# Kernel optimization log

Measured on AMD Instinct MI355X. Metric: run time of the kernel, lower is better.

Reference implementation:

```python
import math
import jax, jax.numpy as jnp
import numpy as np

B, N, DIN, DOUT = 64, 512, 256, 256
EPS = 1e-5  # torch BatchNorm1d default


def setup_inputs() -> dict:
    key = jax.random.key(0)
    k0, k1, k2, k3 = jax.random.split(key, 4)
    x = jax.random.normal(k0, (B, N, DIN), dtype=jnp.float32)
    # row-scaled dense adjacency (keeps activation magnitudes sane)
    adj = jax.random.uniform(k1, (B, N, N), dtype=jnp.float32) / N
    # prefix-style masks: first L_i nodes of each graph are valid
    lengths = jax.random.randint(k2, (B,), N // 4, N + 1)
    mask = (jnp.arange(N)[None, :] < lengths[:, None]).astype(jnp.float32)
    # xavier_normal_ init for weight
    std = math.sqrt(2.0 / (DIN + DOUT))
    weight = jax.random.normal(k3, (DIN, DOUT), dtype=jnp.float32) * std
    bias = jnp.zeros((DOUT,), dtype=jnp.float32)
    gamma = jnp.ones((DOUT,), dtype=jnp.float32)   # BN affine scale
    beta = jnp.zeros((DOUT,), dtype=jnp.float32)   # BN affine shift
    return {"x": x, "adj": adj, "mask": mask, "weight": weight,
            "bias": bias, "gamma": gamma, "beta": beta}


def reference(x, adj, mask, weight, bias, gamma, beta):
    # y = adj @ x @ W + b
    y = jnp.einsum('bnm,bmd->bnd', adj, x)
    y = jnp.einsum('bnd,de->bne', y, weight) + bias
    # masked BatchNorm1d (training mode): batch stats over all valid nodes,
    # equivalent to the torch code's pack -> BN -> unpack on prefix masks.
    m = mask[:, :, None]                       # [B, N, 1]
    n = jnp.sum(mask)                          # total valid nodes
    mean = jnp.sum(y * m, axis=(0, 1)) / n     # [DOUT]
    var = jnp.sum(((y - mean) ** 2) * m, axis=(0, 1)) / n  # biased var
    y = ((y - mean) * jax.lax.rsqrt(var + EPS) * gamma + beta) * m
    return jax.nn.relu(y)
```

## Files before the change

### kernel.cpp

```cpp
#include <hip/hip_runtime.h>

#define B_    64
#define N_    512
#define DIN_  256
#define DOUT_ 256
#define EPS_  1e-5f
#define ROWS_ (B_ * N_)
#define NBLK_Y2 512

typedef __attribute__((ext_vector_type(8))) short bf16x8;
typedef __attribute__((ext_vector_type(8))) unsigned short u16x8;
typedef __attribute__((ext_vector_type(4))) float f32x4;
typedef __attribute__((ext_vector_type(4))) short short4v;

__device__ __forceinline__ short f2bf(float f) {
    unsigned u = __builtin_bit_cast(unsigned, f);
    u += 0x7fff + ((u >> 16) & 1);
    return (short)(u >> 16);
}

__device__ __forceinline__ void gload_lds16(const void* g, void* l) {
    __builtin_amdgcn_global_load_lds(
        (const __attribute__((address_space(1))) void*)g,
        (__attribute__((address_space(3))) void*)l, 16, 0, 0);
}


__global__ __launch_bounds__(256) void wt_cvt(const float* __restrict__ W,
                                              short* __restrict__ WTf) {
    const int c = blockIdx.x * 256 + threadIdx.x;
    const int kf = c >> 10, ef = (c >> 6) & 15, lp = c & 63;
    const int e = ef * 16 + (lp & 15);
    const int k0 = kf * 32 + (lp >> 4) * 8;
    bf16x8 h;
    #pragma unroll
    for (int j = 0; j < 8; ++j)
        h[j] = f2bf(W[(size_t)(k0 + j) * DOUT_ + e]);
    *(bf16x8*)&WTf[(size_t)c * 8] = h;
}

__global__ __launch_bounds__(512, 4) void gemm_xw(const float* __restrict__ X,
                                                  const short* __restrict__ WTf,
                                                  short* __restrict__ xwT) {
    __shared__ __align__(16) short Bs[2][16384];
    __shared__ __align__(16) short As[2][4096];
    const int tid = threadIdx.x, wv = tid >> 6, lane = tid & 63;
    const int lrow = lane & 15, lg = lane >> 4;
    const int bid = blockIdx.x;
    const int rowBase = bid * 64;

    const int s_row = ((tid >> 6) & 3) * 16 + (tid & 15);
    const int s_kloc = (tid >> 8) * 32 + ((tid >> 4) & 3) * 8;
    const float* Xr = &X[(size_t)(rowBase + s_row) * DIN_ + s_kloc];

    f32x4 acc[4][2] = {};
    float4 av0, av1;

    av0 = *(const float4*)(Xr);
    av1 = *(const float4*)(Xr + 4);
    #pragma unroll
    for (int j = 0; j < 4; ++j) {
        int o = tid * 16 + j * 8192;
        gload_lds16((const char*)WTf + o, (char*)&Bs[0][0] + o);
    }
    {
        bf16x8 h = { f2bf(av0.x), f2bf(av0.y), f2bf(av0.z), f2bf(av0.w),
                     f2bf(av1.x), f2bf(av1.y), f2bf(av1.z), f2bf(av1.w) };
        *(bf16x8*)((char*)&As[0][0] + tid * 16) = h;
    }
    __syncthreads();

    int cur = 0;
    for (int c = 0; c < 4; ++c) {
        if (c < 3) {
            av0 = *(const float4*)(Xr + (c + 1) * 64);
            av1 = *(const float4*)(Xr + (c + 1) * 64 + 4);
            #pragma unroll
            for (int j = 0; j < 4; ++j) {
                int o = tid * 16 + j * 8192;
                gload_lds16((const char*)WTf + (c + 1) * 32768 + o,
                            (char*)&Bs[cur ^ 1][0] + o);
            }
        }
        #pragma unroll
        for (int kf2 = 0; kf2 < 2; ++kf2) {
            bf16x8 a[4], b[2];
            #pragma unroll
            for (int m = 0; m < 4; ++m)
                a[m] = *(const bf16x8*)((char*)&As[cur][0] +
                                        ((kf2 * 4 + m) * 64 + lane) * 16);
            #pragma unroll
            for (int nf = 0; nf < 2; ++nf)
                b[nf] = *(const bf16x8*)((char*)&Bs[cur][0] +
                                         ((kf2 * 16 + wv * 2 + nf) * 64 + lane) * 16);
            #pragma unroll
            for (int m = 0; m < 4; ++m)
                #pragma unroll
                for (int nf = 0; nf < 2; ++nf)
                    acc[m][nf] = __builtin_amdgcn_mfma_f32_16x16x32_bf16(
                        a[m], b[nf], acc[m][nf], 0, 0, 0);
        }
        if (c < 3) {
            bf16x8 h = { f2bf(av0.x), f2bf(av0.y), f2bf(av0.z), f2bf(av0.w),
                         f2bf(av1.x), f2bf(av1.y), f2bf(av1.z), f2bf(av1.w) };
            *(bf16x8*)((char*)&As[cur ^ 1][0] + tid * 16) = h;
        }
        __syncthreads();
        cur ^= 1;
    }

    const int bz = bid >> 3, kfbase = (bid & 7) * 2;
    short* xwb = xwT + (size_t)bz * 131072;
    #pragma unroll
    for (int m = 0; m < 4; ++m)
        #pragma unroll
        for (int nf = 0; nf < 2; ++nf) {
            int kf = kfbase + (m >> 1);
            int ef = wv * 2 + nf;
            int lanep = lrow + 16 * ((m & 1) * 2 + (lg >> 1));
            size_t off = ((size_t)(kf * 16 + ef) * 64 + lanep) * 8 + (lg & 1) * 4;
            short4v o = { f2bf(acc[m][nf][0]), f2bf(acc[m][nf][1]),
                          f2bf(acc[m][nf][2]), f2bf(acc[m][nf][3]) };
            *(short4v*)&xwb[off] = o;
        }
}

template <bool BF16Y2>
__global__ __launch_bounds__(512, 4) void gemm_y2(const float* __restrict__ adj,
                                                  const short* __restrict__ xwT,
                                                  const float* __restrict__ bias,
                                                  const float* __restrict__ mask,
                                                  float* __restrict__ outf,
                                                  unsigned short* __restrict__ y2b,
                                                  float* __restrict__ psum,
                                                  float* __restrict__ psumsq,
                                                  float* __restrict__ pcnt) {
    __shared__ __align__(16) short Bs[4][8192];
    __shared__ __align__(16) short As[2][2048];
    const int tid = threadIdx.x, wv = tid >> 6, lane = tid & 63;
    const int lrow = lane & 15, lg = lane >> 4;
    const int bid = blockIdx.x;
    const int swz = ((bid & 7) << 6) | (bid >> 3);
    const int bz = swz >> 3, mt = swz & 7;
    const int rowBase = mt * 64;
    const float* A = adj + (size_t)bz * N_ * N_;
    const short* xwb = xwT + (size_t)bz * 131072;

    const int arow = ((tid >> 7) << 4) | ((tid >> 1) & 15);
    const int akl  = (((tid >> 5) & 3) << 3) | ((tid & 1) << 2);
    const float* Ar = &A[(size_t)(rowBase + arow) * N_ + akl];

    float4 av[2];
    f32x4 acc[4][2] = {};

    float4 av0t = *(const float4*)(Ar);
    av[1] = *(const float4*)(Ar + 32);
    __builtin_amdgcn_sched_barrier(0);
    #pragma unroll
    for (int p = 0; p < 3; ++p) {
        const char* src = (const char*)xwb + p * 16384;
        char* dst = (char*)&Bs[p][0];
        gload_lds16(src + tid * 16, dst + tid * 16);
        gload_lds16(src + tid * 16 + 8192, dst + tid * 16 + 8192);
    }
    __builtin_amdgcn_sched_barrier(0);
    {
        short4v h = { f2bf(av0t.x), f2bf(av0t.y), f2bf(av0t.z), f2bf(av0t.w) };
        *(short4v*)((char*)&As[0][0] + tid * 8) = h;
    }
    asm volatile("s_waitcnt lgkmcnt(0)" ::: "memory");
    asm volatile("s_waitcnt vmcnt(4)" ::: "memory");
    __builtin_amdgcn_s_barrier();
    asm volatile("" ::: "memory");

    #pragma unroll 1
    for (int cc = 0; cc < 16; cc += 4) {
        #pragma unroll
        for (int u = 0; u < 4; ++u) {
            const int c = cc + u;
            {
                const int cn = (c + 2 < 16) ? c + 2 : 15;
                av[c & 1] = *(const float4*)(Ar + cn * 32);
            }
            __builtin_amdgcn_sched_barrier(0);
            {
                const int cn = (c + 3 < 16) ? c + 3 : 15;
                const char* src = (const char*)xwb + cn * 16384;
                char* dst = (char*)&Bs[(c + 3) & 3][0];
                gload_lds16(src + tid * 16, dst + tid * 16);
                gload_lds16(src + tid * 16 + 8192, dst + tid * 16 + 8192);
            }
            __builtin_amdgcn_sched_barrier(0);
            {
                const char* ab = (const char*)&As[c & 1][0];
                const char* bb = (const char*)&Bs[c & 3][0];
                bf16x8 a0 = *(const bf16x8*)(ab + (0 * 64 + lane) * 16);
                bf16x8 a1 = *(const bf16x8*)(ab + (1 * 64 + lane) * 16);
                bf16x8 a2 = *(const bf16x8*)(ab + (2 * 64 + lane) * 16);
                bf16x8 a3 = *(const bf16x8*)(ab + (3 * 64 + lane) * 16);
                bf16x8 b0 = *(const bf16x8*)(bb + ((wv * 2 + 0) * 64 + lane) * 16);
                bf16x8 b1 = *(const bf16x8*)(bb + ((wv * 2 + 1) * 64 + lane) * 16);
                acc[0][0] = __builtin_amdgcn_mfma_f32_16x16x32_bf16(a0, b0, acc[0][0], 0, 0, 0);
                acc[0][1] = __builtin_amdgcn_mfma_f32_16x16x32_bf16(a0, b1, acc[0][1], 0, 0, 0);
                acc[1][0] = __builtin_amdgcn_mfma_f32_16x16x32_bf16(a1, b0, acc[1][0], 0, 0, 0);
                acc[1][1] = __builtin_amdgcn_mfma_f32_16x16x32_bf16(a1, b1, acc[1][1], 0, 0, 0);
                acc[2][0] = __builtin_amdgcn_mfma_f32_16x16x32_bf16(a2, b0, acc[2][0], 0, 0, 0);
                acc[2][1] = __builtin_amdgcn_mfma_f32_16x16x32_bf16(a2, b1, acc[2][1], 0, 0, 0);
                acc[3][0] = __builtin_amdgcn_mfma_f32_16x16x32_bf16(a3, b0, acc[3][0], 0, 0, 0);
                acc[3][1] = __builtin_amdgcn_mfma_f32_16x16x32_bf16(a3, b1, acc[3][1], 0, 0, 0);
            }
            __builtin_amdgcn_sched_barrier(0);
            {
                float4 v = av[(c + 1) & 1];
                short4v h = { f2bf(v.x), f2bf(v.y), f2bf(v.z), f2bf(v.w) };
                *(short4v*)((char*)&As[(c + 1) & 1][0] + tid * 8) = h;
            }
            asm volatile("s_waitcnt lgkmcnt(0)" ::: "memory");
            asm volatile("s_waitcnt vmcnt(5)" ::: "memory");
            __builtin_amdgcn_s_barrier();
            asm volatile("" ::: "memory");
        }
    }

    float* C = outf + (size_t)bz * N_ * DOUT_;
    unsigned short* Cb = y2b + (size_t)bz * N_ * DOUT_;
    float mv[4][4];
    #pragma unroll
    for (int m = 0; m < 4; ++m)
        #pragma unroll
        for (int r = 0; r < 4; ++r)
            mv[m][r] = mask[bz * N_ + rowBase + m * 16 + lg * 4 + r];
    float sv[2] = {0.f, 0.f}, sq[2] = {0.f, 0.f};
    #pragma unroll
    for (int nf = 0; nf < 2; ++nf) {
        const int col = wv * 32 + nf * 16 + lrow;
        const float bv = bias[col];
        #pragma unroll
        for (int m = 0; m < 4; ++m) {
            const int r0 = rowBase + m * 16 + lg * 4;
            #pragma unroll
            for (int r = 0; r < 4; ++r) {
                float v = acc[m][nf][r] + bv;
                if (BF16Y2)
                    Cb[(size_t)(r0 + r) * DOUT_ + col] = (unsigned short)f2bf(v);
                else
                    C[(size_t)(r0 + r) * DOUT_ + col] = v;
                float vm = v * mv[m][r];
                sv[nf] += vm;
                sq[nf] = fmaf(v, vm, sq[nf]);
            }
        }
    }
    #pragma unroll
    for (int nf = 0; nf < 2; ++nf) {
        sv[nf] += __shfl_xor(sv[nf], 16); sv[nf] += __shfl_xor(sv[nf], 32);
        sq[nf] += __shfl_xor(sq[nf], 16); sq[nf] += __shfl_xor(sq[nf], 32);
    }
    const int pidx = bz * 8 + mt;
    if (lg == 0) {
        #pragma unroll
        for (int nf = 0; nf < 2; ++nf) {
            psum[(size_t)pidx * DOUT_ + wv * 32 + nf * 16 + lrow]   = sv[nf];
            psumsq[(size_t)pidx * DOUT_ + wv * 32 + nf * 16 + lrow] = sq[nf];
        }
    }
    if (wv == 0) {
        float cnt = mask[bz * N_ + rowBase + lane];
        #pragma unroll
        for (int i = 1; i < 64; i <<= 1) cnt += __shfl_xor(cnt, i);
        if (lane == 0) pcnt[pidx] = cnt;
    }
}

__global__ __launch_bounds__(256) void finalize2(const float* __restrict__ psum,
                                                 const float* __restrict__ psumsq,
                                                 const float* __restrict__ pcnt,
                                                 const float* __restrict__ gamma,
                                                 const float* __restrict__ beta,
                                                 float* __restrict__ scsh) {
    const int e = blockIdx.x, t = threadIdx.x;
    float s  = psum[(size_t)t * DOUT_ + e]   + psum[(size_t)(t + 256) * DOUT_ + e];
    float ss = psumsq[(size_t)t * DOUT_ + e] + psumsq[(size_t)(t + 256) * DOUT_ + e];
    float n  = pcnt[t] + pcnt[t + 256];
    #pragma unroll
    for (int i = 1; i < 64; i <<= 1) {
        s += __shfl_xor(s, i); ss += __shfl_xor(ss, i); n += __shfl_xor(n, i);
    }
    __shared__ float red[3][4];
    const int wv = t >> 6;
    if ((t & 63) == 0) { red[0][wv] = s; red[1][wv] = ss; red[2][wv] = n; }
    __syncthreads();
    if (t == 0) {
        s  = red[0][0] + red[0][1] + red[0][2] + red[0][3];
        ss = red[1][0] + red[1][1] + red[1][2] + red[1][3];
        n  = red[2][0] + red[2][1] + red[2][2] + red[2][3];
        float mean = s / n;
        float var = ss / n - mean * mean;
        float sc = rsqrtf(var + EPS_) * gamma[e];
        scsh[e] = sc;
        scsh[DOUT_ + e] = beta[e] - mean * sc;
    }
}

__global__ __launch_bounds__(256) void norm_relu_bf(const unsigned short* __restrict__ y2b,
                                                    const float* __restrict__ mask,
                                                    const float* __restrict__ scsh,
                                                    float* __restrict__ out) {
    const int nq = ROWS_ * (DOUT_ / 8);
    for (int q = blockIdx.x * blockDim.x + threadIdx.x; q < nq;
         q += gridDim.x * blockDim.x) {
        int e8 = (q & 31) * 8;
        int r = q >> 5;
        float m = mask[r];
        u16x8 uv = *(const u16x8*)&y2b[(size_t)q * 8];
        float4 sc0 = *(const float4*)&scsh[e8];
        float4 sc1 = *(const float4*)&scsh[e8 + 4];
        float4 sh0 = *(const float4*)&scsh[DOUT_ + e8];
        float4 sh1 = *(const float4*)&scsh[DOUT_ + e8 + 4];
        float4 o0, o1;
        #pragma unroll
        for (int j = 0; j < 4; ++j) {
            float f = __builtin_bit_cast(float, (unsigned)uv[j] << 16);
            (&o0.x)[j] = fmaxf(fmaf(f, (&sc0.x)[j], (&sh0.x)[j]) * m, 0.f);
        }
        #pragma unroll
        for (int j = 0; j < 4; ++j) {
            float f = __builtin_bit_cast(float, (unsigned)uv[j + 4] << 16);
            (&o1.x)[j] = fmaxf(fmaf(f, (&sc1.x)[j], (&sh1.x)[j]) * m, 0.f);
        }
        *(float4*)&out[(size_t)q * 8] = o0;
        *(float4*)&out[(size_t)q * 8 + 4] = o1;
    }
}

__global__ __launch_bounds__(256) void norm_relu_f32(float* __restrict__ y2,
                                                     const float* __restrict__ mask,
                                                     const float* __restrict__ scsh) {
    const int nq = ROWS_ * (DOUT_ / 4);
    for (int q = blockIdx.x * blockDim.x + threadIdx.x; q < nq;
         q += gridDim.x * blockDim.x) {
        int e4 = (q & 63) * 4;
        int r = q >> 6;
        float m = mask[r];
        float4 v  = *(float4*)&y2[(size_t)q * 4];
        float4 sc = *(const float4*)&scsh[e4];
        float4 sh = *(const float4*)&scsh[DOUT_ + e4];
        v.x = fmaxf(fmaf(v.x, sc.x, sh.x) * m, 0.f);
        v.y = fmaxf(fmaf(v.y, sc.y, sh.y) * m, 0.f);
        v.z = fmaxf(fmaf(v.z, sc.z, sh.z) * m, 0.f);
        v.w = fmaxf(fmaf(v.w, sc.w, sh.w) * m, 0.f);
        *(float4*)&y2[(size_t)q * 4] = v;
    }
}

extern "C" void kernel_launch(void* const* d_in, const int* in_sizes, int n_in,
                              void* d_out, int out_size, void* d_ws, size_t ws_size,
                              hipStream_t stream) {
    const float* x      = (const float*)d_in[0];
    const float* adj    = (const float*)d_in[1];
    const float* mask   = (const float*)d_in[2];
    const float* weight = (const float*)d_in[3];
    const float* bias   = (const float*)d_in[4];
    const float* gamma  = (const float*)d_in[5];
    const float* beta   = (const float*)d_in[6];
    float* out = (float*)d_out;

    const size_t xw_elems = (size_t)DOUT_ * ROWS_;
    const size_t need_bf = 131072 + xw_elems * 2 * 2 +
                           (size_t)NBLK_Y2 * DOUT_ * 4 * 2 + NBLK_Y2 * 4 + 2048 + 64;
    const bool use_bf = ws_size >= need_bf;

    short* WTf    = (short*)d_ws;
    short* xwT    = WTf + 256 * 256;
    unsigned short* y2b = (unsigned short*)(xwT + xw_elems);
    float* psum   = use_bf ? (float*)(y2b + xw_elems) : (float*)(y2b);
    float* psumsq = psum + NBLK_Y2 * DOUT_;
    float* pcnt   = psumsq + NBLK_Y2 * DOUT_;
    float* scsh   = pcnt + NBLK_Y2;

    wt_cvt<<<32, 256, 0, stream>>>(weight, WTf);
    gemm_xw<<<512, 512, 0, stream>>>(x, WTf, xwT);
    if (use_bf) {
        gemm_y2<true><<<NBLK_Y2, 512, 0, stream>>>(adj, xwT, bias, mask, out, y2b,
                                                   psum, psumsq, pcnt);
        finalize2<<<256, 256, 0, stream>>>(psum, psumsq, pcnt, gamma, beta, scsh);
        norm_relu_bf<<<2048, 256, 0, stream>>>(y2b, mask, scsh, out);
    } else {
        gemm_y2<false><<<NBLK_Y2, 512, 0, stream>>>(adj, xwT, bias, mask, out, y2b,
                                                    psum, psumsq, pcnt);
        finalize2<<<256, 256, 0, stream>>>(psum, psumsq, pcnt, gamma, beta, scsh);
        norm_relu_f32<<<2048, 256, 0, stream>>>(out, mask, scsh);
    }
}
```

Before: 55.20 us.

## Stage full A tile in LDS upfront and stream B fragments directly from global

Both GEMM kernels now convert and load the entire A row-block (X or adj) into LDS once, with one barrier. B fragments (weights / xw) are then read straight from global memory into registers, one step ahead, instead of going through async LDS staging. This removes the per-step barriers and LDS traffic for B. In exchange it loses the overlap of A loads with compute, and the larger LDS footprint (64KB in gemm_y2) may limit occupancy.

```diff
diff --git a/kernel.cpp b/kernel.cpp
--- a/kernel.cpp
+++ b/kernel.cpp
@@ -19,12 +19,6 @@
     return (short)(u >> 16);
 }
 
-__device__ __forceinline__ void gload_lds16(const void* g, void* l) {
-    __builtin_amdgcn_global_load_lds(
-        (const __attribute__((address_space(1))) void*)g,
-        (__attribute__((address_space(3))) void*)l, 16, 0, 0);
-}
-
 
 __global__ __launch_bounds__(256) void wt_cvt(const float* __restrict__ W,
                                               short* __restrict__ WTf) {
@@ -42,71 +36,51 @@
 __global__ __launch_bounds__(512, 4) void gemm_xw(const float* __restrict__ X,
                                                   const short* __restrict__ WTf,
                                                   short* __restrict__ xwT) {
-    __shared__ __align__(16) short Bs[2][16384];
-    __shared__ __align__(16) short As[2][4096];
+    __shared__ __align__(16) short As[8 * 4 * 64 * 8];
     const int tid = threadIdx.x, wv = tid >> 6, lane = tid & 63;
     const int lrow = lane & 15, lg = lane >> 4;
     const int bid = blockIdx.x;
     const int rowBase = bid * 64;
 
-    const int s_row = ((tid >> 6) & 3) * 16 + (tid & 15);
-    const int s_kloc = (tid >> 8) * 32 + ((tid >> 4) & 3) * 8;
-    const float* Xr = &X[(size_t)(rowBase + s_row) * DIN_ + s_kloc];
-
+    #pragma unroll
+    for (int j = 0; j < 4; ++j) {
+        int s = tid + j * 512;
+        int kf = s >> 8, mf = (s >> 6) & 3, lp = s & 63;
+        int row = mf * 16 + (lp & 15);
+        int k = kf * 32 + (lp >> 4) * 8;
+        const float* src = &X[(size_t)(rowBase + row) * DIN_ + k];
+        float4 v0 = *(const float4*)src;
+        float4 v1 = *(const float4*)(src + 4);
+        bf16x8 h = { f2bf(v0.x), f2bf(v0.y), f2bf(v0.z), f2bf(v0.w),
+                     f2bf(v1.x), f2bf(v1.y), f2bf(v1.z), f2bf(v1.w) };
+        *(bf16x8*)&As[s * 8] = h;
+    }
+    __syncthreads();
+
+    const short* b0p = WTf + ((size_t)(wv * 2 + 0) * 64 + lane) * 8;
+    const short* b1p = WTf + ((size_t)(wv * 2 + 1) * 64 + lane) * 8;
+    bf16x8 bc0 = *(const bf16x8*)(b0p);
+    bf16x8 bc1 = *(const bf16x8*)(b1p);
     f32x4 acc[4][2] = {};
-    float4 av0, av1;
-
-    av0 = *(const float4*)(Xr);
-    av1 = *(const float4*)(Xr + 4);
-    #pragma unroll
-    for (int j = 0; j < 4; ++j) {
-        int o = tid * 16 + j * 8192;
-        gload_lds16((const char*)WTf + o, (char*)&Bs[0][0] + o);
-    }
-    {
-        bf16x8 h = { f2bf(av0.x), f2bf(av0.y), f2bf(av0.z), f2bf(av0.w),
-                     f2bf(av1.x), f2bf(av1.y), f2bf(av1.z), f2bf(av1.w) };
-        *(bf16x8*)((char*)&As[0][0] + tid * 16) = h;
-    }
-    __syncthreads();
-
-    int cur = 0;
-    for (int c = 0; c < 4; ++c) {
-        if (c < 3) {
-            av0 = *(const float4*)(Xr + (c + 1) * 64);
-            av1 = *(const float4*)(Xr + (c + 1) * 64 + 4);
-            #pragma unroll
-            for (int j = 0; j < 4; ++j) {
-                int o = tid * 16 + j * 8192;
-                gload_lds16((const char*)WTf + (c + 1) * 32768 + o,
-                            (char*)&Bs[cur ^ 1][0] + o);
-            }
-        }
-        #pragma unroll
-        for (int kf2 = 0; kf2 < 2; ++kf2) {
-            bf16x8 a[4], b[2];
-            #pragma unroll
-            for (int m = 0; m < 4; ++m)
-                a[m] = *(const bf16x8*)((char*)&As[cur][0] +
-                                        ((kf2 * 4 + m) * 64 + lane) * 16);
-            #pragma unroll
-            for (int nf = 0; nf < 2; ++nf)
-                b[nf] = *(const bf16x8*)((char*)&Bs[cur][0] +
-                                         ((kf2 * 16 + wv * 2 + nf) * 64 + lane) * 16);
-            #pragma unroll
-            for (int m = 0; m < 4; ++m)
-                #pragma unroll
-                for (int nf = 0; nf < 2; ++nf)
-                    acc[m][nf] = __builtin_amdgcn_mfma_f32_16x16x32_bf16(
-                        a[m], b[nf], acc[m][nf], 0, 0, 0);
-        }
-        if (c < 3) {
-            bf16x8 h = { f2bf(av0.x), f2bf(av0.y), f2bf(av0.z), f2bf(av0.w),
-                         f2bf(av1.x), f2bf(av1.y), f2bf(av1.z), f2bf(av1.w) };
-            *(bf16x8*)((char*)&As[cur ^ 1][0] + tid * 16) = h;
-        }
-        __syncthreads();
-        cur ^= 1;
+    #pragma unroll 2
+    for (int c = 0; c < 8; ++c) {
+        const int cn = (c + 1 < 8) ? c + 1 : 7;
+        bf16x8 bn0 = *(const bf16x8*)(b0p + cn * 8192);
+        bf16x8 bn1 = *(const bf16x8*)(b1p + cn * 8192);
+        const short* ab = &As[(c * 256 + lane) * 8];
+        bf16x8 a0 = *(const bf16x8*)(ab);
+        bf16x8 a1 = *(const bf16x8*)(ab + 512);
+        bf16x8 a2 = *(const bf16x8*)(ab + 1024);
+        bf16x8 a3 = *(const bf16x8*)(ab + 1536);
+        acc[0][0] = __builtin_amdgcn_mfma_f32_16x16x32_bf16(a0, bc0, acc[0][0], 0, 0, 0);
+        acc[0][1] = __builtin_amdgcn_mfma_f32_16x16x32_bf16(a0, bc1, acc[0][1], 0, 0, 0);
+        acc[1][0] = __builtin_amdgcn_mfma_f32_16x16x32_bf16(a1, bc0, acc[1][0], 0, 0, 0);
+        acc[1][1] = __builtin_amdgcn_mfma_f32_16x16x32_bf16(a1, bc1, acc[1][1], 0, 0, 0);
+        acc[2][0] = __builtin_amdgcn_mfma_f32_16x16x32_bf16(a2, bc0, acc[2][0], 0, 0, 0);
+        acc[2][1] = __builtin_amdgcn_mfma_f32_16x16x32_bf16(a2, bc1, acc[2][1], 0, 0, 0);
+        acc[3][0] = __builtin_amdgcn_mfma_f32_16x16x32_bf16(a3, bc0, acc[3][0], 0, 0, 0);
+        acc[3][1] = __builtin_amdgcn_mfma_f32_16x16x32_bf16(a3, bc1, acc[3][1], 0, 0, 0);
+        bc0 = bn0; bc1 = bn1;
     }
 
     const int bz = bid >> 3, kfbase = (bid & 7) * 2;
@@ -135,8 +109,7 @@
                                                   float* __restrict__ psum,
                                                   float* __restrict__ psumsq,
                                                   float* __restrict__ pcnt) {
-    __shared__ __align__(16) short Bs[4][8192];
-    __shared__ __align__(16) short As[2][2048];
+    __shared__ __align__(16) short As[16 * 4 * 64 * 8];
     const int tid = threadIdx.x, wv = tid >> 6, lane = tid & 63;
     const int lrow = lane & 15, lg = lane >> 4;
     const int bid = blockIdx.x;
@@ -146,80 +119,45 @@
     const float* A = adj + (size_t)bz * N_ * N_;
     const short* xwb = xwT + (size_t)bz * 131072;
 
-    const int arow = ((tid >> 7) << 4) | ((tid >> 1) & 15);
-    const int akl  = (((tid >> 5) & 3) << 3) | ((tid & 1) << 2);
-    const float* Ar = &A[(size_t)(rowBase + arow) * N_ + akl];
-
-    float4 av[2];
+    #pragma unroll
+    for (int j = 0; j < 8; ++j) {
+        int s = tid + j * 512;
+        int kf = s >> 8, mf = (s >> 6) & 3, lp = s & 63;
+        int row = mf * 16 + (lp & 15);
+        int k = kf * 32 + (lp >> 4) * 8;
+        const float* src = &A[(size_t)(rowBase + row) * N_ + k];
+        float4 v0 = *(const float4*)src;
+        float4 v1 = *(const float4*)(src + 4);
+        bf16x8 h = { f2bf(v0.x), f2bf(v0.y), f2bf(v0.z), f2bf(v0.w),
+                     f2bf(v1.x), f2bf(v1.y), f2bf(v1.z), f2bf(v1.w) };
+        *(bf16x8*)&As[s * 8] = h;
+    }
+    __syncthreads();
+
+    const short* b0p = xwb + ((size_t)(wv * 2 + 0) * 64 + lane) * 8;
+    const short* b1p = xwb + ((size_t)(wv * 2 + 1) * 64 + lane) * 8;
+    bf16x8 bc0 = *(const bf16x8*)(b0p);
+    bf16x8 bc1 = *(const bf16x8*)(b1p);
     f32x4 acc[4][2] = {};
-
-    float4 av0t = *(const float4*)(Ar);
-    av[1] = *(const float4*)(Ar + 32);
-    __builtin_amdgcn_sched_barrier(0);
-    #pragma unroll
-    for (int p = 0; p < 3; ++p) {
-        const char* src = (const char*)xwb + p * 16384;
-        char* dst = (char*)&Bs[p][0];
-        gload_lds16(src + tid * 16, dst + tid * 16);
-        gload_lds16(src + tid * 16 + 8192, dst + tid * 16 + 8192);
-    }
-    __builtin_amdgcn_sched_barrier(0);
-    {
-        short4v h = { f2bf(av0t.x), f2bf(av0t.y), f2bf(av0t.z), f2bf(av0t.w) };
-        *(short4v*)((char*)&As[0][0] + tid * 8) = h;
-    }
-    asm volatile("s_waitcnt lgkmcnt(0)" ::: "memory");
-    asm volatile("s_waitcnt vmcnt(4)" ::: "memory");
-    __builtin_amdgcn_s_barrier();
-    asm volatile("" ::: "memory");
-
-    #pragma unroll 1
-    for (int cc = 0; cc < 16; cc += 4) {
-        #pragma unroll
-        for (int u = 0; u < 4; ++u) {
-            const int c = cc + u;
-            {
-                const int cn = (c + 2 < 16) ? c + 2 : 15;
-                av[c & 1] = *(const float4*)(Ar + cn * 32);
-            }
-            __builtin_amdgcn_sched_barrier(0);
-            {
-                const int cn = (c + 3 < 16) ? c + 3 : 15;
-                const char* src = (const char*)xwb + cn * 16384;
-                char* dst = (char*)&Bs[(c + 3) & 3][0];
-                gload_lds16(src + tid * 16, dst + tid * 16);
-                gload_lds16(src + tid * 16 + 8192, dst + tid * 16 + 8192);
-            }
-            __builtin_amdgcn_sched_barrier(0);
-            {
-                const char* ab = (const char*)&As[c & 1][0];
-                const char* bb = (const char*)&Bs[c & 3][0];
-                bf16x8 a0 = *(const bf16x8*)(ab + (0 * 64 + lane) * 16);
-                bf16x8 a1 = *(const bf16x8*)(ab + (1 * 64 + lane) * 16);
-                bf16x8 a2 = *(const bf16x8*)(ab + (2 * 64 + lane) * 16);
-                bf16x8 a3 = *(const bf16x8*)(ab + (3 * 64 + lane) * 16);
-                bf16x8 b0 = *(const bf16x8*)(bb + ((wv * 2 + 0) * 64 + lane) * 16);
-                bf16x8 b1 = *(const bf16x8*)(bb + ((wv * 2 + 1) * 64 + lane) * 16);
-                acc[0][0] = __builtin_amdgcn_mfma_f32_16x16x32_bf16(a0, b0, acc[0][0], 0, 0, 0);
-                acc[0][1] = __builtin_amdgcn_mfma_f32_16x16x32_bf16(a0, b1, acc[0][1], 0, 0, 0);
-                acc[1][0] = __builtin_amdgcn_mfma_f32_16x16x32_bf16(a1, b0, acc[1][0], 0, 0, 0);
-                acc[1][1] = __builtin_amdgcn_mfma_f32_16x16x32_bf16(a1, b1, acc[1][1], 0, 0, 0);
-                acc[2][0] = __builtin_amdgcn_mfma_f32_16x16x32_bf16(a2, b0, acc[2][0], 0, 0, 0);
-                acc[2][1] = __builtin_amdgcn_mfma_f32_16x16x32_bf16(a2, b1, acc[2][1], 0, 0, 0);
-                acc[3][0] = __builtin_amdgcn_mfma_f32_16x16x32_bf16(a3, b0, acc[3][0], 0, 0, 0);
-                acc[3][1] = __builtin_amdgcn_mfma_f32_16x16x32_bf16(a3, b1, acc[3][1], 0, 0, 0);
-            }
-            __builtin_amdgcn_sched_barrier(0);
-            {
-                float4 v = av[(c + 1) & 1];
-                short4v h = { f2bf(v.x), f2bf(v.y), f2bf(v.z), f2bf(v.w) };
-                *(short4v*)((char*)&As[(c + 1) & 1][0] + tid * 8) = h;
-            }
-            asm volatile("s_waitcnt lgkmcnt(0)" ::: "memory");
-            asm volatile("s_waitcnt vmcnt(5)" ::: "memory");
-            __builtin_amdgcn_s_barrier();
-            asm volatile("" ::: "memory");
-        }
+    #pragma unroll 2
+    for (int c = 0; c < 16; ++c) {
+        const int cn = (c + 1 < 16) ? c + 1 : 15;
+        bf16x8 bn0 = *(const bf16x8*)(b0p + cn * 8192);
+        bf16x8 bn1 = *(const bf16x8*)(b1p + cn * 8192);
+        const short* ab = &As[(c * 256 + lane) * 8];
+        bf16x8 a0 = *(const bf16x8*)(ab);
+        bf16x8 a1 = *(const bf16x8*)(ab + 512);
+        bf16x8 a2 = *(const bf16x8*)(ab + 1024);
+        bf16x8 a3 = *(const bf16x8*)(ab + 1536);
+        acc[0][0] = __builtin_amdgcn_mfma_f32_16x16x32_bf16(a0, bc0, acc[0][0], 0, 0, 0);
+        acc[0][1] = __builtin_amdgcn_mfma_f32_16x16x32_bf16(a0, bc1, acc[0][1], 0, 0, 0);
+        acc[1][0] = __builtin_amdgcn_mfma_f32_16x16x32_bf16(a1, bc0, acc[1][0], 0, 0, 0);
+        acc[1][1] = __builtin_amdgcn_mfma_f32_16x16x32_bf16(a1, bc1, acc[1][1], 0, 0, 0);
+        acc[2][0] = __builtin_amdgcn_mfma_f32_16x16x32_bf16(a2, bc0, acc[2][0], 0, 0, 0);
+        acc[2][1] = __builtin_amdgcn_mfma_f32_16x16x32_bf16(a2, bc1, acc[2][1], 0, 0, 0);
+        acc[3][0] = __builtin_amdgcn_mfma_f32_16x16x32_bf16(a3, bc0, acc[3][0], 0, 0, 0);
+        acc[3][1] = __builtin_amdgcn_mfma_f32_16x16x32_bf16(a3, bc1, acc[3][1], 0, 0, 0);
+        bc0 = bn0; bc1 = bn1;
     }
 
     float* C = outf + (size_t)bz * N_ * DOUT_;
```

Measured after the change: 55.89 us. About the same (+1.3%).
